# Optimization experiments

Hardware: AMD Instinct MI355X
Metric: run time of the kernel (lower is better)

Reference implementation:

```python
import jax, jax.numpy as jnp
import numpy as np

B, S, D, H = 4, 2048, 1024, 16
HD = D // H  # head_dim = 64


def setup_inputs() -> dict:
    key = jax.random.key(0)
    ks = jax.random.split(key, 6)
    scale = 0.02
    x = jax.random.normal(ks[0], (B, S, D), dtype=jnp.float32)
    # per-head projection weights, torch Linear is y = x @ W.T; store as [H, D, HD]
    Wq = jax.random.normal(ks[1], (H, D, HD), dtype=jnp.float32) * scale
    Wk = jax.random.normal(ks[2], (H, D, HD), dtype=jnp.float32) * scale
    Wv = jax.random.normal(ks[3], (H, D, HD), dtype=jnp.float32) * scale
    Wo = jax.random.normal(ks[4], (D, D), dtype=jnp.float32) * scale  # torch [out, in]
    bo = jax.random.normal(ks[5], (D,), dtype=jnp.float32) * scale
    return {"x": x, "Wq": Wq, "Wk": Wk, "Wv": Wv, "Wo": Wo, "bo": bo}


def reference(x, Wq, Wk, Wv, Wo, bo):
    # project: [B,S,D] x [H,D,HD] -> [B,H,S,HD]
    q = jnp.einsum("bsd,hde->bhse", x, Wq)
    k = jnp.einsum("bsd,hde->bhse", x, Wk)
    v = jnp.einsum("bsd,hde->bhse", x, Wv)
    scores = jnp.einsum("bhse,bhte->bhst", q, k) / jnp.sqrt(jnp.float32(HD))
    causal = jnp.tril(jnp.ones((S, S), dtype=bool))  # same as registered tril mask
    scores = jnp.where(causal, scores, -jnp.inf)
    w = jax.nn.softmax(scores, axis=-1)
    out = jnp.einsum("bhst,bhte->bhse", w, v)  # [B,H,S,HD]
    # concat heads along feature dim: [B,S,H*HD] = [B,S,D]
    out = out.transpose(0, 2, 1, 3).reshape(B, S, D)
    # output projection: torch Linear y = x @ W.T + b
    return jnp.einsum("bsd,od->bso", out, Wo) + bo
```

## Files before the change

### kernel.cpp

```cpp
#include <hip/hip_runtime.h>
#include <hip/hip_bf16.h>

typedef __bf16 bf16x8 __attribute__((ext_vector_type(8)));
typedef float f32x4 __attribute__((ext_vector_type(4)));
typedef unsigned short u16x4 __attribute__((ext_vector_type(4)));
typedef unsigned short u16x8 __attribute__((ext_vector_type(8)));
typedef unsigned uint4v __attribute__((ext_vector_type(4)));

#define B_ 4
#define S_ 2048
#define D_ 1024
#define H_ 16
#define HD_ 64

__device__ __forceinline__ unsigned short f2bf(float f) {
  unsigned u = __float_as_uint(f);
  u += 0x7fff + ((u >> 16) & 1);
  return (unsigned short)(u >> 16);
}

__device__ __forceinline__ void gload16(const void* g, void* l) {
  __builtin_amdgcn_global_load_lds((const __attribute__((address_space(1))) unsigned int*)g,
                                   (__attribute__((address_space(3))) unsigned int*)l,
                                   16, 0, 0);
}

__global__ void pack_x_k(const float* __restrict__ in, unsigned short* __restrict__ out, int n4) {
  int i = blockIdx.x * blockDim.x + threadIdx.x;
  int stride = gridDim.x * blockDim.x;
  for (; i < n4; i += stride) {
    float4 v = reinterpret_cast<const float4*>(in)[i];
    u16x4 o = {f2bf(v.x), f2bf(v.y), f2bf(v.z), f2bf(v.w)};
    reinterpret_cast<u16x4*>(out)[i] = o;
  }
}

__global__ void pack_wqkv_k(const float* __restrict__ Wq, const float* __restrict__ Wk,
                            const float* __restrict__ Wv, unsigned short* __restrict__ Wt) {
  int o = blockIdx.x * blockDim.x + threadIdx.x;
  int n = o >> 10;
  int d = o & 1023;
  const float* W = (n < 1024) ? Wq : (n < 2048) ? Wk : Wv;
  int nn = n & 1023;
  int h = nn >> 6, e = nn & 63;
  Wt[o] = f2bf(W[(h << 16) + (d << 6) + e]);
}

__global__ __launch_bounds__(512, 2) void gemm256_k(const unsigned short* __restrict__ A,
                                                    const unsigned short* __restrict__ Bt,
                                                    unsigned short* __restrict__ QK,
                                                    unsigned short* __restrict__ VT,
                                                    int M, int N, int K) {
  __shared__ __align__(16) unsigned short lds[2][3][128 * 64];
  const int tid = threadIdx.x;
  const int wid = tid >> 6, lane = tid & 63;
  const int r = lane & 15, g = lane >> 4;
  const int wm = wid >> 2, wn = wid & 3;

  const int i_hw = blockIdx.y * gridDim.x + blockIdx.x;
  const int xcd = i_hw & 7, j = i_hw >> 3;
  const long arow0 = (long)((xcd & 3) * 8 + (j & 7)) * 256;
  const long bcol0 = (long)((xcd >> 2) * 12 + (j >> 3)) * 128;

  const f32x4 z4 = {0.f, 0.f, 0.f, 0.f};
  f32x4 acc[8][2];
#pragma unroll
  for (int m = 0; m < 8; ++m)
#pragma unroll
    for (int n = 0; n < 2; ++n) acc[m][n] = z4;

  auto stage_half = [&](int kt, int which) {
    const unsigned short* src = (which == 2) ? Bt + bcol0 * K : A + (arow0 + 128 * which) * K;
    const int k0 = kt << 6;
    unsigned short* base = &lds[kt & 1][which][0];
#pragma unroll
    for (int c = 0; c < 2; ++c) {
      const int jj = c * 512 + tid;
      const int row = jj >> 3, cc = jj & 7;
      const int ccs = cc ^ (row & 7);
      gload16(src + (long)row * K + k0 + ccs * 8, base + jj * 8);
    }
  };

  bf16x8 af[4][2], bv[2][2];
  auto read_a = [&](int buf, int mh) {
#pragma unroll
    for (int i2 = 0; i2 < 4; ++i2)
#pragma unroll
      for (int kk = 0; kk < 2; ++kk) {
        const int rowh = (2 * i2 + wm) * 16 + r;
        af[i2][kk] = *(const bf16x8*)&lds[buf][mh][rowh * 64 + (((kk << 2) + g) ^ (rowh & 7)) * 8];
      }
  };
  auto read_b = [&](int buf) {
#pragma unroll
    for (int j2 = 0; j2 < 2; ++j2)
#pragma unroll
      for (int kk = 0; kk < 2; ++kk) {
        const int rowh = (4 * j2 + wn) * 16 + r;
        bv[j2][kk] = *(const bf16x8*)&lds[buf][2][rowh * 64 + (((kk << 2) + g) ^ (rowh & 7)) * 8];
      }
  };
  auto mma_h = [&](int mh) {
    __builtin_amdgcn_s_setprio(1);
#pragma unroll
    for (int kk = 0; kk < 2; ++kk)
#pragma unroll
      for (int i2 = 0; i2 < 4; ++i2)
#pragma unroll
        for (int j2 = 0; j2 < 2; ++j2)
          acc[4 * mh + i2][j2] = __builtin_amdgcn_mfma_f32_16x16x32_bf16(
              af[i2][kk], bv[j2][kk], acc[4 * mh + i2][j2], 0, 0, 0);
    __builtin_amdgcn_s_setprio(0);
  };

  const int nk = K >> 6;
  stage_half(0, 0);
  stage_half(0, 2);
  stage_half(0, 1);
  asm volatile("s_waitcnt vmcnt(2)" ::: "memory");
  asm volatile("s_barrier" ::: "memory");

  for (int t = 0; t < nk; ++t) {
    const int buf = t & 1;
    const bool pre = (t + 1 < nk);
    read_a(buf, 0);
    read_b(buf);
    if (pre) { stage_half(t + 1, 0); stage_half(t + 1, 2); }
    asm volatile("s_barrier" ::: "memory");
    mma_h(0);
    if (pre) asm volatile("s_waitcnt vmcnt(4)" ::: "memory");
    else     asm volatile("s_waitcnt vmcnt(0)" ::: "memory");
    asm volatile("s_waitcnt lgkmcnt(0)\n\ts_barrier" ::: "memory");
    read_a(buf, 1);
    if (pre) stage_half(t + 1, 1);
    asm volatile("s_barrier" ::: "memory");
    mma_h(1);
    if (pre) asm volatile("s_waitcnt vmcnt(2)" ::: "memory");
    asm volatile("s_waitcnt lgkmcnt(0)\n\ts_barrier" ::: "memory");
  }

  if (bcol0 < 2048) {
#pragma unroll
    for (int m = 0; m < 8; ++m)
#pragma unroll
      for (int n = 0; n < 2; ++n)
#pragma unroll
        for (int rr = 0; rr < 4; ++rr) {
          const long row = arow0 + (2 * m + wm) * 16 + g * 4 + rr;
          const long col = bcol0 + (4 * n + wn) * 16 + r;
          QK[row * 2048 + col] = f2bf(acc[m][n][rr]);
        }
  } else {
#pragma unroll
    for (int m = 0; m < 8; ++m) {
      const long row0 = arow0 + (2 * m + wm) * 16 + g * 4;
      const long b = row0 >> 11, s = row0 & 2047;
#pragma unroll
      for (int n = 0; n < 2; ++n) {
        const long vcol = bcol0 - 2048 + (4 * n + wn) * 16 + r;
        const long h = vcol >> 6, e = vcol & 63;
        u16x4 w4;
#pragma unroll
        for (int rr = 0; rr < 4; ++rr) w4[rr] = f2bf(acc[m][n][rr]);
        *(u16x4*)&VT[(((b << 4) + h) * 64 + e) * 2048 + s] = w4;
      }
    }
  }
}

__global__ __launch_bounds__(256, 2) void gemm_bt_k(const unsigned short* __restrict__ A,
                                                    const unsigned short* __restrict__ Bt,
                                                    float* __restrict__ C,
                                                    const float* __restrict__ bias,
                                                    int M, int N, int K) {
  __shared__ __align__(16) unsigned short lA[2][128 * 64];
  __shared__ __align__(16) unsigned short lB[2][128 * 64];
  const int tid = threadIdx.x;
  const int wid = tid >> 6, lane = tid & 63;
  const int r = lane & 15, g = lane >> 4;
  const long arow0 = (long)blockIdx.x * 128;
  const long brow0 = (long)blockIdx.y * 128;
  const int wr = (wid >> 1) * 64, wc = (wid & 1) * 64;

  const f32x4 z4 = {0.f, 0.f, 0.f, 0.f};
  f32x4 acc[4][4];
#pragma unroll
  for (int m = 0; m < 4; ++m)
#pragma unroll
    for (int n = 0; n < 4; ++n) acc[m][n] = z4;

  auto stage = [&](int buf, int k0) {
#pragma unroll
    for (int c = 0; c < 4; ++c) {
      const int j = c * 256 + wid * 64 + lane;
      const int row = j >> 3, col = (j & 7) * 8;
      gload16(A + (arow0 + row) * K + k0 + col, &lA[buf][(c * 256 + wid * 64) * 8]);
      gload16(Bt + (brow0 + row) * K + k0 + col, &lB[buf][(c * 256 + wid * 64) * 8]);
    }
  };

  stage(0, 0);
  __syncthreads();
  const int nk = K >> 6;
  for (int kt = 0; kt < nk; ++kt) {
    const int cur = kt & 1;
    if (kt + 1 < nk) stage(cur ^ 1, (kt + 1) << 6);
#pragma unroll
    for (int kk = 0; kk < 2; ++kk) {
      bf16x8 af[4], bfr[4];
#pragma unroll
      for (int m = 0; m < 4; ++m)
        af[m] = *(const bf16x8*)&lA[cur][(wr + m * 16 + r) * 64 + kk * 32 + g * 8];
#pragma unroll
      for (int n = 0; n < 4; ++n)
        bfr[n] = *(const bf16x8*)&lB[cur][(wc + n * 16 + r) * 64 + kk * 32 + g * 8];
#pragma unroll
      for (int m = 0; m < 4; ++m)
#pragma unroll
        for (int n = 0; n < 4; ++n)
          acc[m][n] = __builtin_amdgcn_mfma_f32_16x16x32_bf16(af[m], bfr[n], acc[m][n], 0, 0, 0);
    }
    __syncthreads();
  }

#pragma unroll
  for (int m = 0; m < 4; ++m) {
#pragma unroll
    for (int n = 0; n < 4; ++n) {
#pragma unroll
      for (int rr = 0; rr < 4; ++rr) {
        const long row = arow0 + wr + m * 16 + g * 4 + rr;
        const long col = brow0 + wc + n * 16 + r;
        C[row * N + col] = acc[m][n][rr] + bias[col];
      }
    }
  }
}

__global__ __launch_bounds__(256, 2) void attn_k(const unsigned short* __restrict__ qk,
                                                 const unsigned short* __restrict__ vt,
                                                 unsigned short* __restrict__ out) {
  __shared__ __align__(16) unsigned short lK[2][64 * 64];
  __shared__ __align__(16) unsigned short lVt[2][64 * 64];

  const int tid = threadIdx.x, wid = tid >> 6, lane = tid & 63;
  const int r = lane & 15, g = lane >> 4;
  const int bh = blockIdx.x;
  const int b = bh >> 4, h = bh & 15;
  const int qb = 15 - (int)blockIdx.y;
  const int q0 = qb * 128;

  const unsigned short* Qg = qk + ((long)b * S_) * 2048 + h * 64;
  const unsigned short* Kg = Qg + 1024;
  const unsigned short* Vg = vt + ((long)(b * 16 + h)) * 64 * 2048;

  int qrow[2];
  bf16x8 qf[2][2];
#pragma unroll
  for (int qs = 0; qs < 2; ++qs) {
    qrow[qs] = q0 + qs * 64 + wid * 16 + r;
#pragma unroll
    for (int kk = 0; kk < 2; ++kk)
      qf[qs][kk] = *(const bf16x8*)&Qg[(long)qrow[qs] * 2048 + kk * 32 + g * 8];
  }

  const f32x4 z4 = {0.f, 0.f, 0.f, 0.f};
  f32x4 o[2][4];
#pragma unroll
  for (int qs = 0; qs < 2; ++qs)
#pragma unroll
    for (int nt = 0; nt < 4; ++nt) o[qs][nt] = z4;
  float m_i[2] = {-1e30f, -1e30f};
  float l_i[2] = {0.f, 0.f};

  auto stage = [&](int buf, int t0) {
#pragma unroll
    for (int c = 0; c < 2; ++c) {
      const int j = c * 256 + tid;
      const int row = j >> 3, cc = j & 7;
      const int ccs = (cc ^ (row & 7)) << 3;
      gload16(Kg + (long)(t0 + row) * 2048 + ccs, &lK[buf][j * 8]);
      gload16(Vg + (long)row * 2048 + t0 + ccs, &lVt[buf][j * 8]);
    }
  };

  const int ntiles = (q0 >> 6) + 2;
  stage(0, 0);

  for (int t = 0; t < ntiles; ++t) {
    const int cur = t & 1;
    __syncthreads();
    if (t + 1 < ntiles) stage(cur ^ 1, (t + 1) << 6);

    const int t0 = t << 6;
    const bool act0 = (t < ntiles - 1);
    const bool diag0 = (t == ntiles - 2);
    const bool diag1 = (t == ntiles - 1);

    f32x4 st[2][4];
#pragma unroll
    for (int tt = 0; tt < 4; ++tt) { st[0][tt] = z4; st[1][tt] = z4; }
    __builtin_amdgcn_s_setprio(1);
#pragma unroll
    for (int kk = 0; kk < 2; ++kk)
#pragma unroll
      for (int tt = 0; tt < 4; ++tt) {
        const int row = tt * 16 + r, cc = kk * 4 + g;
        bf16x8 kf = *(const bf16x8*)&lK[cur][(row * 8 + (cc ^ (row & 7))) * 8];
        st[1][tt] = __builtin_amdgcn_mfma_f32_16x16x32_bf16(kf, qf[1][kk], st[1][tt], 0, 0, 0);
        if (act0)
          st[0][tt] = __builtin_amdgcn_mfma_f32_16x16x32_bf16(kf, qf[0][kk], st[0][tt], 0, 0, 0);
      }
    __builtin_amdgcn_s_setprio(0);

    bf16x8 pf[2][2];
    unsigned corr_bits[2] = {0x3f800000u, 0x3f800000u};
    bool dodef[2] = {true, true};
#pragma unroll
    for (int qs = 0; qs < 2; ++qs) {
      if (qs == 0 && !act0) continue;
      const bool diag = qs ? diag1 : diag0;
      float sv[16];
#pragma unroll
      for (int tt = 0; tt < 4; ++tt)
#pragma unroll
        for (int rg = 0; rg < 4; ++rg) {
          float s = st[qs][tt][rg];
          if (diag && (t0 + tt * 16 + g * 4 + rg > qrow[qs])) s = -1e30f;
          sv[tt * 4 + rg] = s;
        }
      float h0 = fmaxf(fmaxf(fmaxf(sv[0], sv[1]), fmaxf(sv[2], sv[3])),
                       fmaxf(fmaxf(sv[4], sv[5]), fmaxf(sv[6], sv[7])));
      float h1 = fmaxf(fmaxf(fmaxf(sv[8], sv[9]), fmaxf(sv[10], sv[11])),
                       fmaxf(fmaxf(sv[12], sv[13]), fmaxf(sv[14], sv[15])));
      const float pmax = fmaxf(h0, h1);
      const bool defer = __all(pmax - m_i[qs] <= 64.f);
      float corr = 1.f;
      if (!defer) {
        float mx = fmaxf(pmax, m_i[qs]);
        mx = fmaxf(mx, __shfl_xor(mx, 16, 64));
        mx = fmaxf(mx, __shfl_xor(mx, 32, 64));
        corr = __expf((m_i[qs] - mx) * 0.125f);
        m_i[qs] = mx;
      }
      dodef[qs] = defer;
      corr_bits[qs] = __float_as_uint(corr);
      const float m8 = m_i[qs] * 0.125f;
      float p[16];
      float rs = 0.f;
#pragma unroll
      for (int i = 0; i < 16; ++i) {
        p[i] = __expf(__builtin_fmaf(sv[i], 0.125f, -m8));
        rs += p[i];
      }
      rs += __shfl_xor(rs, 16, 64);
      rs += __shfl_xor(rs, 32, 64);
      l_i[qs] = l_i[qs] * corr + rs;
      unsigned cw[4][2];
#pragma unroll
      for (int tt = 0; tt < 4; ++tt)
#pragma unroll
        for (int e = 0; e < 2; ++e)
          asm("v_cvt_pk_bf16_f32 %0, %1, %2"
              : "=v"(cw[tt][e]) : "v"(p[tt * 4 + 2 * e]), "v"(p[tt * 4 + 2 * e + 1]));
#pragma unroll
      for (int kk = 0; kk < 2; ++kk) {
        unsigned x0 = cw[2 * kk][0], y0 = cw[2 * kk + 1][0];
        unsigned x1 = cw[2 * kk][1], y1 = cw[2 * kk + 1][1];
        asm volatile("v_permlane32_swap_b32 %0, %1" : "+v"(x0), "+v"(y0));
        asm volatile("v_permlane16_swap_b32 %0, %1" : "+v"(x0), "+v"(y0));
        asm volatile("v_permlane32_swap_b32 %0, %1" : "+v"(x1), "+v"(y1));
        asm volatile("v_permlane16_swap_b32 %0, %1" : "+v"(x1), "+v"(y1));
        uint4v w = {x0, x1, y0, y1};
        pf[qs][kk] = *(bf16x8*)&w;
      }
    }
#pragma unroll
    for (int qs = 0; qs < 2; ++qs) {
      if (qs == 0 && !act0) continue;
      if (!dodef[qs]) {
        const float corr = __uint_as_float(corr_bits[qs]);
#pragma unroll
        for (int rr = 0; rr < 4; ++rr) {
          const float c = __shfl(corr, g * 4 + rr, 64);
#pragma unroll
          for (int nt = 0; nt < 4; ++nt) o[qs][nt][rr] *= c;
        }
      }
    }

    __builtin_amdgcn_s_setprio(1);
#pragma unroll
    for (int kk = 0; kk < 2; ++kk)
#pragma unroll
      for (int nt = 0; nt < 4; ++nt) {
        const int row = nt * 16 + r, cc = kk * 4 + g;
        const bf16x8 vf = *(const bf16x8*)&lVt[cur][(row * 8 + (cc ^ (row & 7))) * 8];
        o[1][nt] = __builtin_amdgcn_mfma_f32_16x16x32_bf16(pf[1][kk], vf, o[1][nt], 0, 0, 0);
        if (act0)
          o[0][nt] = __builtin_amdgcn_mfma_f32_16x16x32_bf16(pf[0][kk], vf, o[0][nt], 0, 0, 0);
      }
    __builtin_amdgcn_s_setprio(0);
  }

#pragma unroll
  for (int qs = 0; qs < 2; ++qs) {
    float linv[4];
#pragma unroll
    for (int rr = 0; rr < 4; ++rr)
      linv[rr] = 1.f / __shfl(l_i[qs], g * 4 + rr, 64);
#pragma unroll
    for (int nt = 0; nt < 4; ++nt)
#pragma unroll
      for (int rr = 0; rr < 4; ++rr) {
        const long s = q0 + qs * 64 + wid * 16 + g * 4 + rr;
        out[((long)b * S_ + s) * 1024 + h * 64 + nt * 16 + r] = f2bf(o[qs][nt][rr] * linv[rr]);
      }
  }
}

extern "C" void kernel_launch(void* const* d_in, const int* in_sizes, int n_in,
                              void* d_out, int out_size, void* d_ws, size_t ws_size,
                              hipStream_t stream) {
  const float* x = (const float*)d_in[0];
  const float* Wq = (const float*)d_in[1];
  const float* Wk = (const float*)d_in[2];
  const float* Wv = (const float*)d_in[3];
  const float* Wo = (const float*)d_in[4];
  const float* bo = (const float*)d_in[5];
  float* out = (float*)d_out;

  char* ws = (char*)d_ws;
  unsigned short* Xb = (unsigned short*)(ws);
  unsigned short* Wt = (unsigned short*)(ws + (16ul << 20));
  unsigned short* Wob = (unsigned short*)(ws + (22ul << 20));
  unsigned short* QK = (unsigned short*)(ws + (24ul << 20));
  unsigned short* VT = (unsigned short*)(ws + (56ul << 20));
  unsigned short* AO = (unsigned short*)(ws + (72ul << 20));

  pack_x_k<<<2048, 256, 0, stream>>>(x, Xb, (B_ * S_ * D_) / 4);
  pack_x_k<<<512, 256, 0, stream>>>(Wo, Wob, (D_ * D_) / 4);
  pack_wqkv_k<<<(3 * D_ * D_) / 256, 256, 0, stream>>>(Wq, Wk, Wv, Wt);

  gemm256_k<<<dim3(32, 24), 512, 0, stream>>>(Xb, Wt, QK, VT, B_ * S_, 3 * D_, D_);
  attn_k<<<dim3(64, 16), 256, 0, stream>>>(QK, VT, AO);
  gemm_bt_k<<<dim3(64, 8), 256, 0, stream>>>(AO, Wob, out, bo, B_ * S_, D_, D_);
}
```

Measured before the change: 192.1 us.

## Widen QKV GEMM tile to 256x192 and reuse 256x128 pipelined kernel for output projection

The fused QKV projection GEMM grows its per-block tile from 256x128 to 256x192. This cuts the grid from 768 to 512 blocks, a single wave at two blocks per CU, and raises MFMA work per A-tile load. The epilogue now decides per column group whether to write to QK or to the transposed V. The output projection drops the simpler 128x128 double-buffered kernel for a new 512-thread, 256x128 kernel with the same XCD-aware tile mapping and split-half software pipeline. Risks include more LDS per block (about 112KB for the QKV kernel, which may limit occupancy) and more accumulator registers.

```diff
diff --git a/kernel.cpp b/kernel.cpp
--- a/kernel.cpp
+++ b/kernel.cpp
@@ -51,7 +51,9 @@
                                                     unsigned short* __restrict__ QK,
                                                     unsigned short* __restrict__ VT,
                                                     int M, int N, int K) {
-  __shared__ __align__(16) unsigned short lds[2][3][128 * 64];
+  __shared__ __align__(16) unsigned short lA0[2][128 * 64];
+  __shared__ __align__(16) unsigned short lA1[2][128 * 64];
+  __shared__ __align__(16) unsigned short lB[2][192 * 64];
   const int tid = threadIdx.x;
   const int wid = tid >> 6, lane = tid & 63;
   const int r = lane & 15, g = lane >> 4;
@@ -60,21 +62,22 @@
   const int i_hw = blockIdx.y * gridDim.x + blockIdx.x;
   const int xcd = i_hw & 7, j = i_hw >> 3;
   const long arow0 = (long)((xcd & 3) * 8 + (j & 7)) * 256;
-  const long bcol0 = (long)((xcd >> 2) * 12 + (j >> 3)) * 128;
+  const long bcol0 = (long)((xcd >> 2) * 8 + (j >> 3)) * 192;
 
   const f32x4 z4 = {0.f, 0.f, 0.f, 0.f};
-  f32x4 acc[8][2];
+  f32x4 acc[8][3];
 #pragma unroll
   for (int m = 0; m < 8; ++m)
 #pragma unroll
-    for (int n = 0; n < 2; ++n) acc[m][n] = z4;
+    for (int n = 0; n < 3; ++n) acc[m][n] = z4;
 
   auto stage_half = [&](int kt, int which) {
     const unsigned short* src = (which == 2) ? Bt + bcol0 * K : A + (arow0 + 128 * which) * K;
     const int k0 = kt << 6;
-    unsigned short* base = &lds[kt & 1][which][0];
-#pragma unroll
-    for (int c = 0; c < 2; ++c) {
+    unsigned short* base = (which == 0) ? &lA0[kt & 1][0]
+                         : (which == 1) ? &lA1[kt & 1][0] : &lB[kt & 1][0];
+    const int nch = (which == 2) ? 3 : 2;
+    for (int c = 0; c < nch; ++c) {
       const int jj = c * 512 + tid;
       const int row = jj >> 3, cc = jj & 7;
       const int ccs = cc ^ (row & 7);
@@ -82,23 +85,23 @@
     }
   };
 
-  bf16x8 af[4][2], bv[2][2];
-  auto read_a = [&](int buf, int mh) {
+  bf16x8 af[4][2], bv[3][2];
+  auto read_a = [&](const unsigned short* lbase) {
 #pragma unroll
     for (int i2 = 0; i2 < 4; ++i2)
 #pragma unroll
       for (int kk = 0; kk < 2; ++kk) {
         const int rowh = (2 * i2 + wm) * 16 + r;
-        af[i2][kk] = *(const bf16x8*)&lds[buf][mh][rowh * 64 + (((kk << 2) + g) ^ (rowh & 7)) * 8];
+        af[i2][kk] = *(const bf16x8*)&lbase[rowh * 64 + (((kk << 2) + g) ^ (rowh & 7)) * 8];
       }
   };
   auto read_b = [&](int buf) {
 #pragma unroll
-    for (int j2 = 0; j2 < 2; ++j2)
+    for (int j2 = 0; j2 < 3; ++j2)
 #pragma unroll
       for (int kk = 0; kk < 2; ++kk) {
         const int rowh = (4 * j2 + wn) * 16 + r;
-        bv[j2][kk] = *(const bf16x8*)&lds[buf][2][rowh * 64 + (((kk << 2) + g) ^ (rowh & 7)) * 8];
+        bv[j2][kk] = *(const bf16x8*)&lB[buf][rowh * 64 + (((kk << 2) + g) ^ (rowh & 7)) * 8];
       }
   };
   auto mma_h = [&](int mh) {
@@ -108,7 +111,7 @@
 #pragma unroll
       for (int i2 = 0; i2 < 4; ++i2)
 #pragma unroll
-        for (int j2 = 0; j2 < 2; ++j2)
+        for (int j2 = 0; j2 < 3; ++j2)
           acc[4 * mh + i2][j2] = __builtin_amdgcn_mfma_f32_16x16x32_bf16(
               af[i2][kk], bv[j2][kk], acc[4 * mh + i2][j2], 0, 0, 0);
     __builtin_amdgcn_s_setprio(0);
@@ -124,7 +127,131 @@
   for (int t = 0; t < nk; ++t) {
     const int buf = t & 1;
     const bool pre = (t + 1 < nk);
-    read_a(buf, 0);
+    read_a(&lA0[buf][0]);
+    read_b(buf);
+    if (pre) { stage_half(t + 1, 0); stage_half(t + 1, 2); }
+    asm volatile("s_barrier" ::: "memory");
+    mma_h(0);
+    if (pre) asm volatile("s_waitcnt vmcnt(5)" ::: "memory");
+    else     asm volatile("s_waitcnt vmcnt(0)" ::: "memory");
+    asm volatile("s_waitcnt lgkmcnt(0)\n\ts_barrier" ::: "memory");
+    read_a(&lA1[buf][0]);
+    if (pre) stage_half(t + 1, 1);
+    asm volatile("s_barrier" ::: "memory");
+    mma_h(1);
+    if (pre) asm volatile("s_waitcnt vmcnt(2)" ::: "memory");
+    asm volatile("s_waitcnt lgkmcnt(0)\n\ts_barrier" ::: "memory");
+  }
+
+#pragma unroll
+  for (int j2 = 0; j2 < 3; ++j2) {
+    const long colb = bcol0 + (4 * j2 + wn) * 16;
+    if (colb < 2048) {
+#pragma unroll
+      for (int m = 0; m < 8; ++m)
+#pragma unroll
+        for (int rr = 0; rr < 4; ++rr) {
+          const long row = arow0 + (2 * m + wm) * 16 + g * 4 + rr;
+          QK[row * 2048 + colb + r] = f2bf(acc[m][j2][rr]);
+        }
+    } else {
+      const long vcol = colb - 2048 + r;
+      const long h = vcol >> 6, e = vcol & 63;
+#pragma unroll
+      for (int m = 0; m < 8; ++m) {
+        const long row0 = arow0 + (2 * m + wm) * 16 + g * 4;
+        const long b = row0 >> 11, s = row0 & 2047;
+        u16x4 w4;
+#pragma unroll
+        for (int rr = 0; rr < 4; ++rr) w4[rr] = f2bf(acc[m][j2][rr]);
+        *(u16x4*)&VT[(((b << 4) + h) * 64 + e) * 2048 + s] = w4;
+      }
+    }
+  }
+}
+
+__global__ __launch_bounds__(512, 2) void gemm_op_k(const unsigned short* __restrict__ A,
+                                                    const unsigned short* __restrict__ Bt,
+                                                    float* __restrict__ C,
+                                                    const float* __restrict__ bias,
+                                                    int M, int N, int K) {
+  __shared__ __align__(16) unsigned short lA0[2][128 * 64];
+  __shared__ __align__(16) unsigned short lA1[2][128 * 64];
+  __shared__ __align__(16) unsigned short lB[2][128 * 64];
+  const int tid = threadIdx.x;
+  const int wid = tid >> 6, lane = tid & 63;
+  const int r = lane & 15, g = lane >> 4;
+  const int wm = wid >> 2, wn = wid & 3;
+
+  const int i_hw = blockIdx.y * gridDim.x + blockIdx.x;
+  const int xcd = i_hw & 7, j = i_hw >> 3;
+  const long arow0 = (long)((xcd & 3) * 8 + (j & 7)) * 256;
+  const long bcol0 = (long)((xcd >> 2) * 4 + (j >> 3)) * 128;
+
+  const f32x4 z4 = {0.f, 0.f, 0.f, 0.f};
+  f32x4 acc[8][2];
+#pragma unroll
+  for (int m = 0; m < 8; ++m)
+#pragma unroll
+    for (int n = 0; n < 2; ++n) acc[m][n] = z4;
+
+  auto stage_half = [&](int kt, int which) {
+    const unsigned short* src = (which == 2) ? Bt + bcol0 * K : A + (arow0 + 128 * which) * K;
+    const int k0 = kt << 6;
+    unsigned short* base = (which == 0) ? &lA0[kt & 1][0]
+                         : (which == 1) ? &lA1[kt & 1][0] : &lB[kt & 1][0];
+#pragma unroll
+    for (int c = 0; c < 2; ++c) {
+      const int jj = c * 512 + tid;
+      const int row = jj >> 3, cc = jj & 7;
+      const int ccs = cc ^ (row & 7);
+      gload16(src + (long)row * K + k0 + ccs * 8, base + jj * 8);
+    }
+  };
+
+  bf16x8 af[4][2], bv[2][2];
+  auto read_a = [&](const unsigned short* lbase) {
+#pragma unroll
+    for (int i2 = 0; i2 < 4; ++i2)
+#pragma unroll
+      for (int kk = 0; kk < 2; ++kk) {
+        const int rowh = (2 * i2 + wm) * 16 + r;
+        af[i2][kk] = *(const bf16x8*)&lbase[rowh * 64 + (((kk << 2) + g) ^ (rowh & 7)) * 8];
+      }
+  };
+  auto read_b = [&](int buf) {
+#pragma unroll
+    for (int j2 = 0; j2 < 2; ++j2)
+#pragma unroll
+      for (int kk = 0; kk < 2; ++kk) {
+        const int rowh = (4 * j2 + wn) * 16 + r;
+        bv[j2][kk] = *(const bf16x8*)&lB[buf][rowh * 64 + (((kk << 2) + g) ^ (rowh & 7)) * 8];
+      }
+  };
+  auto mma_h = [&](int mh) {
+    __builtin_amdgcn_s_setprio(1);
+#pragma unroll
+    for (int kk = 0; kk < 2; ++kk)
+#pragma unroll
+      for (int i2 = 0; i2 < 4; ++i2)
+#pragma unroll
+        for (int j2 = 0; j2 < 2; ++j2)
+          acc[4 * mh + i2][j2] = __builtin_amdgcn_mfma_f32_16x16x32_bf16(
+              af[i2][kk], bv[j2][kk], acc[4 * mh + i2][j2], 0, 0, 0);
+    __builtin_amdgcn_s_setprio(0);
+  };
+
+  const int nk = K >> 6;
+  stage_half(0, 0);
+  stage_half(0, 2);
+  stage_half(0, 1);
+  asm volatile("s_waitcnt vmcnt(2)" ::: "memory");
+  asm volatile("s_barrier" ::: "memory");
+
+  for (int t = 0; t < nk; ++t) {
+    const int buf = t & 1;
+    const bool pre = (t + 1 < nk);
+    read_a(&lA0[buf][0]);
     read_b(buf);
     if (pre) { stage_half(t + 1, 0); stage_half(t + 1, 2); }
     asm volatile("s_barrier" ::: "memory");
@@ -132,7 +259,7 @@
     if (pre) asm volatile("s_waitcnt vmcnt(4)" ::: "memory");
     else     asm volatile("s_waitcnt vmcnt(0)" ::: "memory");
     asm volatile("s_waitcnt lgkmcnt(0)\n\ts_barrier" ::: "memory");
-    read_a(buf, 1);
+    read_a(&lA1[buf][0]);
     if (pre) stage_half(t + 1, 1);
     asm volatile("s_barrier" ::: "memory");
     mma_h(1);
@@ -140,102 +267,16 @@
     asm volatile("s_waitcnt lgkmcnt(0)\n\ts_barrier" ::: "memory");
   }
 
-  if (bcol0 < 2048) {
-#pragma unroll
-    for (int m = 0; m < 8; ++m)
-#pragma unroll
-      for (int n = 0; n < 2; ++n)
-#pragma unroll
-        for (int rr = 0; rr < 4; ++rr) {
-          const long row = arow0 + (2 * m + wm) * 16 + g * 4 + rr;
-          const long col = bcol0 + (4 * n + wn) * 16 + r;
-          QK[row * 2048 + col] = f2bf(acc[m][n][rr]);
-        }
-  } else {
-#pragma unroll
-    for (int m = 0; m < 8; ++m) {
-      const long row0 = arow0 + (2 * m + wm) * 16 + g * 4;
-      const long b = row0 >> 11, s = row0 & 2047;
-#pragma unroll
-      for (int n = 0; n < 2; ++n) {
-        const long vcol = bcol0 - 2048 + (4 * n + wn) * 16 + r;
-        const long h = vcol >> 6, e = vcol & 63;
-        u16x4 w4;
-#pragma unroll
-        for (int rr = 0; rr < 4; ++rr) w4[rr] = f2bf(acc[m][n][rr]);
-        *(u16x4*)&VT[(((b << 4) + h) * 64 + e) * 2048 + s] = w4;
-      }
-    }
-  }
-}
-
-__global__ __launch_bounds__(256, 2) void gemm_bt_k(const unsigned short* __restrict__ A,
-                                                    const unsigned short* __restrict__ Bt,
-                                                    float* __restrict__ C,
-                                                    const float* __restrict__ bias,
-                                                    int M, int N, int K) {
-  __shared__ __align__(16) unsigned short lA[2][128 * 64];
-  __shared__ __align__(16) unsigned short lB[2][128 * 64];
-  const int tid = threadIdx.x;
-  const int wid = tid >> 6, lane = tid & 63;
-  const int r = lane & 15, g = lane >> 4;
-  const long arow0 = (long)blockIdx.x * 128;
-  const long brow0 = (long)blockIdx.y * 128;
-  const int wr = (wid >> 1) * 64, wc = (wid & 1) * 64;
-
-  const f32x4 z4 = {0.f, 0.f, 0.f, 0.f};
-  f32x4 acc[4][4];
-#pragma unroll
-  for (int m = 0; m < 4; ++m)
-#pragma unroll
-    for (int n = 0; n < 4; ++n) acc[m][n] = z4;
-
-  auto stage = [&](int buf, int k0) {
-#pragma unroll
-    for (int c = 0; c < 4; ++c) {
-      const int j = c * 256 + wid * 64 + lane;
-      const int row = j >> 3, col = (j & 7) * 8;
-      gload16(A + (arow0 + row) * K + k0 + col, &lA[buf][(c * 256 + wid * 64) * 8]);
-      gload16(Bt + (brow0 + row) * K + k0 + col, &lB[buf][(c * 256 + wid * 64) * 8]);
-    }
-  };
-
-  stage(0, 0);
-  __syncthreads();
-  const int nk = K >> 6;
-  for (int kt = 0; kt < nk; ++kt) {
-    const int cur = kt & 1;
-    if (kt + 1 < nk) stage(cur ^ 1, (kt + 1) << 6);
-#pragma unroll
-    for (int kk = 0; kk < 2; ++kk) {
-      bf16x8 af[4], bfr[4];
-#pragma unroll
-      for (int m = 0; m < 4; ++m)
-        af[m] = *(const bf16x8*)&lA[cur][(wr + m * 16 + r) * 64 + kk * 32 + g * 8];
-#pragma unroll
-      for (int n = 0; n < 4; ++n)
-        bfr[n] = *(const bf16x8*)&lB[cur][(wc + n * 16 + r) * 64 + kk * 32 + g * 8];
-#pragma unroll
-      for (int m = 0; m < 4; ++m)
-#pragma unroll
-        for (int n = 0; n < 4; ++n)
-          acc[m][n] = __builtin_amdgcn_mfma_f32_16x16x32_bf16(af[m], bfr[n], acc[m][n], 0, 0, 0);
-    }
-    __syncthreads();
-  }
-
-#pragma unroll
-  for (int m = 0; m < 4; ++m) {
-#pragma unroll
-    for (int n = 0; n < 4; ++n) {
+#pragma unroll
+  for (int m = 0; m < 8; ++m)
+#pragma unroll
+    for (int n = 0; n < 2; ++n)
 #pragma unroll
       for (int rr = 0; rr < 4; ++rr) {
-        const long row = arow0 + wr + m * 16 + g * 4 + rr;
-        const long col = brow0 + wc + n * 16 + r;
+        const long row = arow0 + (2 * m + wm) * 16 + g * 4 + rr;
+        const long col = bcol0 + (4 * n + wn) * 16 + r;
         C[row * N + col] = acc[m][n][rr] + bias[col];
       }
-    }
-  }
 }
 
 __global__ __launch_bounds__(256, 2) void attn_k(const unsigned short* __restrict__ qk,
@@ -443,7 +484,7 @@
   pack_x_k<<<512, 256, 0, stream>>>(Wo, Wob, (D_ * D_) / 4);
   pack_wqkv_k<<<(3 * D_ * D_) / 256, 256, 0, stream>>>(Wq, Wk, Wv, Wt);
 
-  gemm256_k<<<dim3(32, 24), 512, 0, stream>>>(Xb, Wt, QK, VT, B_ * S_, 3 * D_, D_);
+  gemm256_k<<<dim3(32, 16), 512, 0, stream>>>(Xb, Wt, QK, VT, B_ * S_, 3 * D_, D_);
   attn_k<<<dim3(64, 16), 256, 0, stream>>>(QK, VT, AO);
-  gemm_bt_k<<<dim3(64, 8), 256, 0, stream>>>(AO, Wob, out, bo, B_ * S_, D_, D_);
-}
+  gemm_op_k<<<dim3(32, 8), 512, 0, stream>>>(AO, Wob, out, bo, B_ * S_, D_, D_);
+}
```

Measured after the change: 178.8 us. 1.07x faster.
